# Optimization experiments

Hardware: AMD Instinct MI355X
Metric: run time of the kernel (lower is better)

## Reference

```python
import jax, jax.numpy as jnp
import numpy as np

NUM_HEADS = 16
BN_EPS = 1e-3  # tf.layers.BatchNormalization default epsilon


def _z_norm(a, axis, scale):
    mu = jnp.mean(a, axis=axis, keepdims=True)
    sd = jnp.std(a, axis=axis, keepdims=True)
    return (a - mu) / (sd * scale + 1e-10)


def setup_inputs() -> dict:
    key = jax.random.key(0)
    ks = jax.random.split(key, 12)
    B, S, D = 4, 1024, 1024
    w = lambda k: jax.random.normal(k, (D, D), dtype=jnp.float32) * 0.02
    return {
        'q': jax.random.normal(ks[0], (B, S, D), dtype=jnp.float32),
        'k': jax.random.normal(ks[1], (B, S, D), dtype=jnp.float32),
        'v': jax.random.normal(ks[2], (B, S, D), dtype=jnp.float32),
        'mask': jax.random.randint(ks[3], (B, 1, S, S), 0, 2, dtype=jnp.int32),
        'is_training': 0,
        'q_gamma': jnp.ones((D,), jnp.float32),
        'q_beta': jnp.zeros((D,), jnp.float32),
        'q_mean': jax.random.normal(ks[4], (D,), dtype=jnp.float32) * 0.1,
        'q_var': jnp.ones((D,), jnp.float32),
        'Wq': w(ks[5]), 'bq': jnp.zeros((D,), jnp.float32),
        'Wqq': w(ks[6]), 'bqq': jnp.zeros((D,), jnp.float32),
        'Wo': w(ks[7]), 'bo': jnp.zeros((D,), jnp.float32),
    }


def reference(q, k, v, mask, is_training, q_gamma, q_beta, q_mean, q_var,
              Wq, bq, Wqq, bqq, Wo, bo):
    B, S, D = q.shape
    H = NUM_HEADS
    dh = D // H
    # BatchNorm (inference mode: call() passes no training flag -> moving stats)
    x = (q - q_mean) * jax.lax.rsqrt(q_var + BN_EPS) * q_gamma + q_beta
    # q = wqq(relu(wq(.)))  (k/v projections are dead: call() sets k = v = q)
    x = jax.nn.relu(x @ Wq + bq)
    x = x @ Wqq + bqq
    qh = x.reshape(B, S, H, dh).transpose(0, 2, 1, 3)  # [B,H,S,dh]
    logits = jnp.einsum('bhqd,bhkd->bhqk', qh, qh) / jnp.sqrt(jnp.float32(dh))
    logits = logits + mask.astype(logits.dtype) * -1e9
    attn = jax.nn.softmax(logits, axis=3)  # [B,H,S,S]
    last = jnp.mean(logits, axis=-1, keepdims=True)        # [B,H,S,1]
    last2 = jnp.mean(logits, axis=(2, 3), keepdims=True)   # [B,H,1,1]
    w_within = jax.nn.softmax(_z_norm(last, 2, 2), axis=2)   # softmax over queries
    w_betw = jax.nn.softmax(_z_norm(last2, 1, 2), axis=1)    # softmax over heads
    attn = attn * w_within * w_betw
    out = jnp.einsum('bhqk,bhkd->bhqd', attn, qh)           # v == qh
    out = out.transpose(0, 2, 1, 3).reshape(B, S, D)
    out = out @ Wo + bo
    return out, attn
```

## Files before the change

### kernel.cpp

```cpp
#include <hip/hip_runtime.h>
#include <math.h>


constexpr int Bz = 4, S = 1024, D = 1024, H = 16, DH = 64;
constexpr int N_ROWS = Bz * S;
#define BN_EPS 1e-3f
#define NEG_BIG -1e9f

typedef __attribute__((ext_vector_type(8))) short bf16x8;
typedef __attribute__((ext_vector_type(8))) unsigned short u16x8;
typedef __attribute__((ext_vector_type(4))) float f32x4;

__device__ inline unsigned short f2bf(float f) {
  union { float f; unsigned int u; } v; v.f = f;
  unsigned int u = v.u;
  return (unsigned short)((u + 0x7FFFu + ((u >> 16) & 1u)) >> 16);
}
__device__ inline float bf2f(unsigned short h) {
  union { unsigned int u; float f; } v; v.u = ((unsigned int)h) << 16;
  return v.f;
}
__device__ inline bf16x8 pack8(float4 a, float4 b) {
  bf16x8 v;
  v[0] = (short)f2bf(a.x); v[1] = (short)f2bf(a.y);
  v[2] = (short)f2bf(a.z); v[3] = (short)f2bf(a.w);
  v[4] = (short)f2bf(b.x); v[5] = (short)f2bf(b.y);
  v[6] = (short)f2bf(b.z); v[7] = (short)f2bf(b.w);
  return v;
}
__device__ inline float4 bnf(float4 f, float4 s, float4 sh) {
  return make_float4(fmaf(f.x, s.x, sh.x), fmaf(f.y, s.y, sh.y),
                     fmaf(f.z, s.z, sh.z), fmaf(f.w, s.w, sh.w));
}

__global__ __launch_bounds__(256)
void k_prep_all(const float* __restrict__ W0, const float* __restrict__ W1,
                const float* __restrict__ W2, unsigned short* __restrict__ T0,
                unsigned short* __restrict__ T1, unsigned short* __restrict__ T2,
                const float* __restrict__ gamma, const float* __restrict__ beta,
                const float* __restrict__ mean, const float* __restrict__ var,
                float* __restrict__ bnsc, float* __restrict__ bnsh,
                const int* __restrict__ mask, float* __restrict__ n_cnt2,
                float* __restrict__ cs) {
  __shared__ float Ls[64][65];
  const int bid = blockIdx.x, t = threadIdx.x;
  if (bid < 768) {
    const int z = bid >> 8, rem = bid & 255;
    const float* W = z == 0 ? W0 : (z == 1 ? W1 : W2);
    unsigned short* T = z == 0 ? T0 : (z == 1 ? T1 : T2);
    const int k0 = (rem & 15) * 64, n0 = (rem >> 4) * 64;
    {
      const int r = t >> 2, c0 = (t & 3) * 16;
#pragma unroll
      for (int i = 0; i < 4; ++i) {
        float4 f = *(const float4*)&W[(size_t)(k0 + r) * 1024 + n0 + c0 + 4 * i];
        Ls[r][c0 + 4 * i] = f.x; Ls[r][c0 + 4 * i + 1] = f.y;
        Ls[r][c0 + 4 * i + 2] = f.z; Ls[r][c0 + 4 * i + 3] = f.w;
      }
    }
    __syncthreads();
    {
      const int d = t >> 2, c = t & 3;
      u16x8 o0, o1;
#pragma unroll
      for (int i = 0; i < 8; ++i) {
        o0[i] = f2bf(Ls[c * 16 + i][d]);
        o1[i] = f2bf(Ls[c * 16 + 8 + i][d]);
      }
      unsigned short* dst = &T[(size_t)(n0 + d) * 1024 + k0 + c * 16];
      *(u16x8*)dst = o0;
      *(u16x8*)(dst + 8) = o1;
    }
  } else if (bid < 832) {
    const int id = bid - 768;
    const int row = id * 64 + (t >> 2);
    const int4* mp = (const int4*)&mask[(size_t)row * 1024 + (t & 3) * 256];
    int s = 0;
#pragma unroll 8
    for (int i = 0; i < 64; ++i) { int4 m = mp[i]; s += (m.x + m.y) + (m.z + m.w); }
    s += __shfl_xor(s, 1, 64);
    s += __shfl_xor(s, 2, 64);
    if ((t & 3) == 0) n_cnt2[row] = (float)s;
  } else if (bid < 836) {
    const int id = bid - 832;
    *(float4*)&cs[id * 1024 + t * 4] = make_float4(0.f, 0.f, 0.f, 0.f);
  } else {
    const int i = (bid - 836) * 256 + t;
    float sc = gamma[i] * rsqrtf(var[i] + BN_EPS);
    bnsc[i] = sc;
    bnsh[i] = beta[i] - mean[i] * sc;
  }
}

template<int AMODE, bool RELU, bool OUTBF, bool CSUM>
__global__ __launch_bounds__(256)
void k_gemm2n(const void* __restrict__ Asrc, const unsigned short* __restrict__ BT,
              const float* __restrict__ bias, void* __restrict__ C,
              const float* __restrict__ bnsc, const float* __restrict__ bnsh,
              float* __restrict__ cs) {
  __shared__ unsigned short As[128 * 64];
  __shared__ unsigned short Bs[64 * 64];
  const int t = threadIdx.x;
  const int w = t >> 6, l = t & 63, l15 = l & 15, l4 = l >> 4;
  const int m0 = blockIdx.x * 128, n0 = blockIdx.y * 64;
  const int wm = (w >> 1) * 64, wn = (w & 1) * 32;

  f32x4 acc[4][2];
#pragma unroll
  for (int i = 0; i < 4; ++i)
#pragma unroll
    for (int j = 0; j < 2; ++j) acc[i][j] = (f32x4){0.f, 0.f, 0.f, 0.f};

  for (int k0 = 0; k0 < 1024; k0 += 64) {
    __syncthreads();
#pragma unroll
    for (int i = 0; i < 4; ++i) {
      const int c = i * 256 + t, row = c >> 3, slot = c & 7;
      bf16x8 v;
      if (AMODE == 0) {
        v = *(const bf16x8*)&((const unsigned short*)Asrc)[(size_t)(m0 + row) * 1024 + k0 + slot * 8];
      } else {
        const float* ap = &((const float*)Asrc)[(size_t)(m0 + row) * 1024 + k0 + slot * 8];
        float4 f0 = *(const float4*)ap, f1 = *(const float4*)(ap + 4);
        float4 s0 = *(const float4*)&bnsc[k0 + slot * 8];
        float4 s1 = *(const float4*)&bnsc[k0 + slot * 8 + 4];
        float4 h0 = *(const float4*)&bnsh[k0 + slot * 8];
        float4 h1 = *(const float4*)&bnsh[k0 + slot * 8 + 4];
        v = pack8(bnf(f0, s0, h0), bnf(f1, s1, h1));
      }
      *(bf16x8*)((char*)As + row * 128 + ((slot * 16) ^ ((row & 7) << 4))) = v;
    }
#pragma unroll
    for (int i = 0; i < 2; ++i) {
      const int c = i * 256 + t, row = c >> 3, slot = c & 7;
      bf16x8 v = *(const bf16x8*)&BT[(size_t)(n0 + row) * 1024 + k0 + slot * 8];
      *(bf16x8*)((char*)Bs + row * 128 + ((slot * 16) ^ ((row & 7) << 4))) = v;
    }
    __syncthreads();
    bf16x8 af[4][2], bfr[2][2];
#pragma unroll
    for (int bm = 0; bm < 4; ++bm) {
      const int r = wm + bm * 16 + l15;
#pragma unroll
      for (int kk = 0; kk < 2; ++kk)
        af[bm][kk] = *(const bf16x8*)((const char*)As + r * 128 +
                                      ((kk * 64 + l4 * 16) ^ ((r & 7) << 4)));
    }
#pragma unroll
    for (int bn = 0; bn < 2; ++bn) {
      const int r = wn + bn * 16 + l15;
#pragma unroll
      for (int kk = 0; kk < 2; ++kk)
        bfr[bn][kk] = *(const bf16x8*)((const char*)Bs + r * 128 +
                                       ((kk * 64 + l4 * 16) ^ ((r & 7) << 4)));
    }
#pragma unroll
    for (int bm = 0; bm < 4; ++bm)
#pragma unroll
      for (int bn = 0; bn < 2; ++bn) {
        acc[bm][bn] = __builtin_amdgcn_mfma_f32_16x16x32_bf16(af[bm][0], bfr[bn][0], acc[bm][bn], 0, 0, 0);
        acc[bm][bn] = __builtin_amdgcn_mfma_f32_16x16x32_bf16(af[bm][1], bfr[bn][1], acc[bm][bn], 0, 0, 0);
      }
  }
  float bv[2];
#pragma unroll
  for (int bn = 0; bn < 2; ++bn) bv[bn] = bias[n0 + wn + bn * 16 + l15];
  float csum[2] = {0.f, 0.f};
#pragma unroll
  for (int bm = 0; bm < 4; ++bm)
#pragma unroll
    for (int bn = 0; bn < 2; ++bn)
#pragma unroll
      for (int r = 0; r < 4; ++r) {
        float v = acc[bm][bn][r] + bv[bn];
        if (RELU) v = fmaxf(v, 0.f);
        if (CSUM) csum[bn] += v;
        const size_t idx = (size_t)(m0 + wm + bm * 16 + l4 * 4 + r) * 1024 +
                           n0 + wn + bn * 16 + l15;
        if (OUTBF) ((unsigned short*)C)[idx] = f2bf(v);
        else ((float*)C)[idx] = v;
      }
  if (CSUM) {
#pragma unroll
    for (int bn = 0; bn < 2; ++bn) {
      float s = csum[bn];
      s += __shfl_xor(s, 16, 64);
      s += __shfl_xor(s, 32, 64);
      if (l4 == 0)
        atomicAdd(&cs[(m0 >> 10) * 1024 + n0 + wn + bn * 16 + l15], s);
    }
  }
}

__global__ __launch_bounds__(256)
void k_cvt(const unsigned short* __restrict__ xqb, unsigned short* __restrict__ qhT) {
  __shared__ unsigned short Ls[64][72];
  const int t = threadIdx.x;
  const int b = blockIdx.x >> 4;
  const int sb = (blockIdx.x & 15) * 64;
  const int h = blockIdx.y;
  {
    const int r = t >> 2, c0 = (t & 3) * 16;
    const unsigned short* src = &xqb[(size_t)(b * 1024 + sb + r) * 1024 + h * 64 + c0];
    u16x8 a = *(const u16x8*)src;
    u16x8 b8 = *(const u16x8*)(src + 8);
    *(u16x8*)&Ls[r][c0] = a;
    *(u16x8*)&Ls[r][c0 + 8] = b8;
  }
  __syncthreads();
  {
    const int d = t >> 2, c = t & 3;
    u16x8 o0, o1;
#pragma unroll
    for (int i = 0; i < 8; ++i) {
      o0[i] = Ls[c * 16 + i][d];
      o1[i] = Ls[c * 16 + 8 + i][d];
    }
    unsigned short* dst = &qhT[(size_t)((b * 16 + h) * 64 + d) * 1024 + sb + c * 16];
    *(u16x8*)dst = o0;
    *(u16x8*)(dst + 8) = o1;
  }
}

template<int PASS>
__global__ __launch_bounds__(256)
void k_attn5(const unsigned short* __restrict__ xqb, const int* __restrict__ mask,
             const unsigned short* __restrict__ qhT, const float* __restrict__ w_row,
             float* __restrict__ attn, unsigned short* __restrict__ pvb,
             float* __restrict__ denom) {
  __shared__ unsigned short Ks[2][64 * 64];
  __shared__ unsigned short Pst[PASS ? 4 * 16 * 64 : 8];

  const int t = threadIdx.x;
  const int w = t >> 6, l = t & 63;
  const int l15 = l & 15, l4 = l >> 4;
  const int q0 = blockIdx.x * 64;
  const int h = blockIdx.y, b = blockIdx.z;
  const int bh = b * 16 + h;

  bf16x8 qa0, qa1;
  {
    const unsigned short* qp =
        &xqb[(size_t)(b * 1024 + q0 + w * 16 + l15) * 1024 + h * 64 + l4 * 8];
    qa0 = *(const bf16x8*)qp;
    qa1 = *(const bf16x8*)(qp + 32);
  }

  float wsc[4];
  if (PASS == 1) {
#pragma unroll
    for (int r = 0; r < 4; ++r)
      wsc[r] = w_row[(size_t)bh * 1024 + q0 + w * 16 + l4 * 4 + r];
  }

  float dsum[4] = {0.f, 0.f, 0.f, 0.f};
  f32x4 vacc[4];
#pragma unroll
  for (int c = 0; c < 4; ++c) vacc[c] = (f32x4){0.f, 0.f, 0.f, 0.f};

  const int srow = t >> 3, sslot = t & 7;
  const int sswz = (sslot * 16) ^ ((srow & 7) << 4);
  const size_t sga = (size_t)(b * 1024 + srow) * 1024 + h * 64 + sslot * 8;

  bf16x8 s0 = *(const bf16x8*)&xqb[sga];
  bf16x8 s1 = *(const bf16x8*)&xqb[sga + 32 * 1024];
  *(bf16x8*)((char*)Ks[0] + srow * 128 + sswz) = s0;
  *(bf16x8*)((char*)Ks[0] + (srow + 32) * 128 + sswz) = s1;
  s0 = *(const bf16x8*)&xqb[sga + 64 * 1024];
  s1 = *(const bf16x8*)&xqb[sga + 96 * 1024];

  for (int ti = 0; ti < 16; ++ti) {
    __syncthreads();
    const int cur = ti & 1;
    if (ti < 15) {
      *(bf16x8*)((char*)Ks[cur ^ 1] + srow * 128 + sswz) = s0;
      *(bf16x8*)((char*)Ks[cur ^ 1] + (srow + 32) * 128 + sswz) = s1;
    }
    if (ti < 14) {
      s0 = *(const bf16x8*)&xqb[sga + (size_t)(ti + 2) * 65536];
      s1 = *(const bf16x8*)&xqb[sga + (size_t)(ti + 2) * 65536 + 32 * 1024];
    }
    const int k0 = ti * 64;

    f32x4 lacc[4];
#pragma unroll
    for (int c = 0; c < 4; ++c) {
      const int r = c * 16 + l15;
      const char* kb = (const char*)Ks[cur] + r * 128;
      const int rsw = (r & 7) << 4;
      bf16x8 kb0 = *(const bf16x8*)(kb + ((l4 * 16) ^ rsw));
      bf16x8 kb1 = *(const bf16x8*)(kb + ((64 + l4 * 16) ^ rsw));
      f32x4 z = (f32x4){0.f, 0.f, 0.f, 0.f};
      z = __builtin_amdgcn_mfma_f32_16x16x32_bf16(qa0, kb0, z, 0, 0, 0);
      z = __builtin_amdgcn_mfma_f32_16x16x32_bf16(qa1, kb1, z, 0, 0, 0);
      lacc[c] = z;
    }

    int mrr[4][4];
#pragma unroll
    for (int c = 0; c < 4; ++c)
#pragma unroll
      for (int r = 0; r < 4; ++r)
        mrr[c][r] = mask[(size_t)(b * 1024 + q0 + w * 16 + l4 * 4 + r) * 1024 +
                         k0 + c * 16 + l15];

#pragma unroll
    for (int c = 0; c < 4; ++c) {
#pragma unroll
      for (int r = 0; r < 4; ++r) {
        float p = __expf(fmaf((float)mrr[c][r], NEG_BIG, lacc[c][r] * 0.125f));
        if (PASS == 0) {
          dsum[r] += p;
        } else {
          attn[(size_t)(bh * 1024 + q0 + w * 16 + l4 * 4 + r) * 1024 +
               k0 + c * 16 + l15] = p * wsc[r];
          const int qq = l4 * 4 + r;
          *(unsigned short*)((char*)&Pst[w * 1024] + qq * 128 +
                             (((c * 16 + l15) * 2) ^ ((qq & 7) << 4))) = f2bf(p);
        }
      }
    }

    if (PASS == 1) {
#pragma unroll
      for (int kk = 0; kk < 2; ++kk) {
        const char* pb = (const char*)&Pst[w * 1024] + l15 * 128;
        bf16x8 pa = *(const bf16x8*)(pb + ((kk * 64 + l4 * 16) ^ ((l15 & 7) << 4)));
#pragma unroll
        for (int c = 0; c < 4; ++c) {
          bf16x8 vb = *(const bf16x8*)&qhT[(size_t)(bh * 64 + c * 16 + l15) * 1024 +
                                           k0 + kk * 32 + l4 * 8];
          vacc[c] = __builtin_amdgcn_mfma_f32_16x16x32_bf16(pa, vb, vacc[c], 0, 0, 0);
        }
      }
    }
  }

  if (PASS == 0) {
#pragma unroll
    for (int r = 0; r < 4; ++r) {
      float d2 = dsum[r];
#pragma unroll
      for (int m = 1; m < 16; m <<= 1) d2 += __shfl_xor(d2, m, 64);
      if (l15 == 0)
        denom[(size_t)bh * 1024 + q0 + w * 16 + l4 * 4 + r] = d2;
    }
  } else {
#pragma unroll
    for (int c = 0; c < 4; ++c)
#pragma unroll
      for (int r = 0; r < 4; ++r)
        pvb[(size_t)(b * 1024 + q0 + w * 16 + l4 * 4 + r) * 1024 +
            h * 64 + c * 16 + l15] = f2bf(vacc[c][r] * wsc[r]);
  }
}

__global__ __launch_bounds__(256)
void k_wwithin(const unsigned short* __restrict__ xqb, const float* __restrict__ cs,
               const float* __restrict__ n_cnt2, const float* __restrict__ denom,
               float* __restrict__ w_row) {
  __shared__ double buf[1024];
  __shared__ double red[256];
  __shared__ float csl[64];
  __shared__ double sh_mu, sh_sd, sh_zm, sh_es;
  const int bh = blockIdx.x, t = threadIdx.x;
  const int base = bh << 10;
  const int b = bh >> 4, h = bh & 15;
  const int nbase = b << 10;
  if (t < 64) csl[t] = cs[b * 1024 + h * 64 + t];
  __syncthreads();
  double part = 0;
  for (int j = 0; j < 4; ++j) {
    const int q2 = t + j * 256;
    const unsigned short* xr = &xqb[(size_t)(b * 1024 + q2) * 1024 + h * 64];
    float s = 0.f;
#pragma unroll
    for (int dd = 0; dd < 64; dd += 8) {
      u16x8 xv = *(const u16x8*)&xr[dd];
      s += bf2f(xv[0]) * csl[dd]     + bf2f(xv[1]) * csl[dd + 1] +
           bf2f(xv[2]) * csl[dd + 2] + bf2f(xv[3]) * csl[dd + 3] +
           bf2f(xv[4]) * csl[dd + 4] + bf2f(xv[5]) * csl[dd + 5] +
           bf2f(xv[6]) * csl[dd + 6] + bf2f(xv[7]) * csl[dd + 7];
    }
    double last = ((double)(s * 0.125f) - 1e9 * (double)n_cnt2[nbase + q2]) * (1.0 / 1024.0);
    buf[q2] = last; part += last;
  }
  red[t] = part; __syncthreads();
  for (int s2 = 128; s2 > 0; s2 >>= 1) { if (t < s2) red[t] += red[t + s2]; __syncthreads(); }
  if (t == 0) sh_mu = red[0] * (1.0 / 1024.0);
  __syncthreads();
  const double mu = sh_mu;
  part = 0;
  for (int q2 = t; q2 < 1024; q2 += 256) { double d = buf[q2] - mu; part += d * d; }
  red[t] = part; __syncthreads();
  for (int s2 = 128; s2 > 0; s2 >>= 1) { if (t < s2) red[t] += red[t + s2]; __syncthreads(); }
  if (t == 0) sh_sd = sqrt(red[0] * (1.0 / 1024.0));
  __syncthreads();
  const double dn = sh_sd * 2.0 + 1e-10;
  part = -1e300;
  for (int q2 = t; q2 < 1024; q2 += 256) {
    double z = (buf[q2] - mu) / dn;
    buf[q2] = z;
    part = fmax(part, z);
  }
  red[t] = part; __syncthreads();
  for (int s2 = 128; s2 > 0; s2 >>= 1) { if (t < s2) red[t] = fmax(red[t], red[t + s2]); __syncthreads(); }
  if (t == 0) sh_zm = red[0];
  __syncthreads();
  const double zm = sh_zm;
  part = 0;
  for (int q2 = t; q2 < 1024; q2 += 256) {
    double e = exp(buf[q2] - zm);
    buf[q2] = e; part += e;
  }
  red[t] = part; __syncthreads();
  for (int s2 = 128; s2 > 0; s2 >>= 1) { if (t < s2) red[t] += red[t + s2]; __syncthreads(); }
  if (t == 0) sh_es = red[0];
  __syncthreads();
  const double tot = sh_es;
  for (int q2 = t; q2 < 1024; q2 += 256) {
    w_row[base + q2] = (float)(buf[q2] / tot * 0.0625 / (double)denom[base + q2]);
  }
}

extern "C" void kernel_launch(void* const* d_in, const int* in_sizes, int n_in,
                              void* d_out, int out_size, void* d_ws, size_t ws_size,
                              hipStream_t stream) {
  const float* q      = (const float*)d_in[0];
  const int*   mask   = (const int*)d_in[3];
  const float* q_gamma = (const float*)d_in[5];
  const float* q_beta  = (const float*)d_in[6];
  const float* q_mean  = (const float*)d_in[7];
  const float* q_var   = (const float*)d_in[8];
  const float* Wq  = (const float*)d_in[9];
  const float* bq  = (const float*)d_in[10];
  const float* Wqq = (const float*)d_in[11];
  const float* bqq = (const float*)d_in[12];
  const float* Wo  = (const float*)d_in[13];
  const float* bo  = (const float*)d_in[14];

  float* out  = (float*)d_out;
  float* attn = (float*)d_out + (size_t)N_ROWS * D;
  unsigned short* xqb = (unsigned short*)d_out;

  char* ws = (char*)d_ws;
  unsigned short* x1b = (unsigned short*)(ws);
  unsigned short* qhT = (unsigned short*)(ws + (8u << 20));
  unsigned short* pvb = (unsigned short*)(ws + (16u << 20));
  unsigned short* WqT  = (unsigned short*)(ws + (32u << 20));
  unsigned short* WqqT = (unsigned short*)(ws + (34u << 20));
  unsigned short* WoT  = (unsigned short*)(ws + (36u << 20));
  float* cs     = (float*)(ws + (38u << 20));
  float* denom  = cs + 4096;
  float* w_row  = denom + 65536;
  float* n_cnt2 = w_row + 65536;
  float* bnsc   = n_cnt2 + 4096;
  float* bnsh   = bnsc + 1024;

  k_prep_all<<<840, 256, 0, stream>>>(Wq, Wqq, Wo, WqT, WqqT, WoT,
                                      q_gamma, q_beta, q_mean, q_var, bnsc, bnsh,
                                      mask, n_cnt2, cs);

  dim3 gg(32, 16);
  k_gemm2n<1, true, true, false><<<gg, 256, 0, stream>>>(q, WqT, bq, x1b, bnsc, bnsh, nullptr);
  k_gemm2n<0, false, true, true><<<gg, 256, 0, stream>>>(x1b, WqqT, bqq, xqb, nullptr, nullptr, cs);

  k_cvt<<<dim3(64, 16), 256, 0, stream>>>(xqb, qhT);

  dim3 ga(16, 16, 4);
  k_attn5<0><<<ga, 256, 0, stream>>>(xqb, mask, nullptr, nullptr, nullptr, nullptr, denom);
  k_wwithin<<<Bz * H, 256, 0, stream>>>(xqb, cs, n_cnt2, denom, w_row);
  k_attn5<1><<<ga, 256, 0, stream>>>(xqb, mask, qhT, w_row, attn, pvb, nullptr);

  k_gemm2n<0, false, false, false><<<gg, 256, 0, stream>>>(pvb, WoT, bo, out, nullptr, nullptr, nullptr);
}
```

Baseline: 247.4 us.

## Fuse two-pass attention into single pass with full-row probabilities staged in LDS

Replaces the two attention passes (one for the softmax denominator, one for the weighted output) with a single kernel. It keeps the whole 64x1024 bf16 probability tile in shared memory, finishes the normalisation after the loop, then writes attn from LDS with coalesced float4 stores. The within-query weight is now computed independently of the denominator, which removes the recomputation of QK^T, exp and the mask reads from the first pass. In exchange it uses 128KB of LDS per block, so only one block fits per CU. K tiles are now read straight from global memory instead of double-buffered LDS. attn values are also rounded through bf16 before they are written.

```diff
diff --git a/kernel.cpp b/kernel.cpp
--- a/kernel.cpp
+++ b/kernel.cpp
@@ -9,6 +9,7 @@
 
 typedef __attribute__((ext_vector_type(8))) short bf16x8;
 typedef __attribute__((ext_vector_type(8))) unsigned short u16x8;
+typedef __attribute__((ext_vector_type(4))) unsigned short u16x4;
 typedef __attribute__((ext_vector_type(4))) float f32x4;
 
 __device__ inline unsigned short f2bf(float f) {
@@ -222,143 +223,9 @@
   }
 }
 
-template<int PASS>
 __global__ __launch_bounds__(256)
-void k_attn5(const unsigned short* __restrict__ xqb, const int* __restrict__ mask,
-             const unsigned short* __restrict__ qhT, const float* __restrict__ w_row,
-             float* __restrict__ attn, unsigned short* __restrict__ pvb,
-             float* __restrict__ denom) {
-  __shared__ unsigned short Ks[2][64 * 64];
-  __shared__ unsigned short Pst[PASS ? 4 * 16 * 64 : 8];
-
-  const int t = threadIdx.x;
-  const int w = t >> 6, l = t & 63;
-  const int l15 = l & 15, l4 = l >> 4;
-  const int q0 = blockIdx.x * 64;
-  const int h = blockIdx.y, b = blockIdx.z;
-  const int bh = b * 16 + h;
-
-  bf16x8 qa0, qa1;
-  {
-    const unsigned short* qp =
-        &xqb[(size_t)(b * 1024 + q0 + w * 16 + l15) * 1024 + h * 64 + l4 * 8];
-    qa0 = *(const bf16x8*)qp;
-    qa1 = *(const bf16x8*)(qp + 32);
-  }
-
-  float wsc[4];
-  if (PASS == 1) {
-#pragma unroll
-    for (int r = 0; r < 4; ++r)
-      wsc[r] = w_row[(size_t)bh * 1024 + q0 + w * 16 + l4 * 4 + r];
-  }
-
-  float dsum[4] = {0.f, 0.f, 0.f, 0.f};
-  f32x4 vacc[4];
-#pragma unroll
-  for (int c = 0; c < 4; ++c) vacc[c] = (f32x4){0.f, 0.f, 0.f, 0.f};
-
-  const int srow = t >> 3, sslot = t & 7;
-  const int sswz = (sslot * 16) ^ ((srow & 7) << 4);
-  const size_t sga = (size_t)(b * 1024 + srow) * 1024 + h * 64 + sslot * 8;
-
-  bf16x8 s0 = *(const bf16x8*)&xqb[sga];
-  bf16x8 s1 = *(const bf16x8*)&xqb[sga + 32 * 1024];
-  *(bf16x8*)((char*)Ks[0] + srow * 128 + sswz) = s0;
-  *(bf16x8*)((char*)Ks[0] + (srow + 32) * 128 + sswz) = s1;
-  s0 = *(const bf16x8*)&xqb[sga + 64 * 1024];
-  s1 = *(const bf16x8*)&xqb[sga + 96 * 1024];
-
-  for (int ti = 0; ti < 16; ++ti) {
-    __syncthreads();
-    const int cur = ti & 1;
-    if (ti < 15) {
-      *(bf16x8*)((char*)Ks[cur ^ 1] + srow * 128 + sswz) = s0;
-      *(bf16x8*)((char*)Ks[cur ^ 1] + (srow + 32) * 128 + sswz) = s1;
-    }
-    if (ti < 14) {
-      s0 = *(const bf16x8*)&xqb[sga + (size_t)(ti + 2) * 65536];
-      s1 = *(const bf16x8*)&xqb[sga + (size_t)(ti + 2) * 65536 + 32 * 1024];
-    }
-    const int k0 = ti * 64;
-
-    f32x4 lacc[4];
-#pragma unroll
-    for (int c = 0; c < 4; ++c) {
-      const int r = c * 16 + l15;
-      const char* kb = (const char*)Ks[cur] + r * 128;
-      const int rsw = (r & 7) << 4;
-      bf16x8 kb0 = *(const bf16x8*)(kb + ((l4 * 16) ^ rsw));
-      bf16x8 kb1 = *(const bf16x8*)(kb + ((64 + l4 * 16) ^ rsw));
-      f32x4 z = (f32x4){0.f, 0.f, 0.f, 0.f};
-      z = __builtin_amdgcn_mfma_f32_16x16x32_bf16(qa0, kb0, z, 0, 0, 0);
-      z = __builtin_amdgcn_mfma_f32_16x16x32_bf16(qa1, kb1, z, 0, 0, 0);
-      lacc[c] = z;
-    }
-
-    int mrr[4][4];
-#pragma unroll
-    for (int c = 0; c < 4; ++c)
-#pragma unroll
-      for (int r = 0; r < 4; ++r)
-        mrr[c][r] = mask[(size_t)(b * 1024 + q0 + w * 16 + l4 * 4 + r) * 1024 +
-                         k0 + c * 16 + l15];
-
-#pragma unroll
-    for (int c = 0; c < 4; ++c) {
-#pragma unroll
-      for (int r = 0; r < 4; ++r) {
-        float p = __expf(fmaf((float)mrr[c][r], NEG_BIG, lacc[c][r] * 0.125f));
-        if (PASS == 0) {
-          dsum[r] += p;
-        } else {
-          attn[(size_t)(bh * 1024 + q0 + w * 16 + l4 * 4 + r) * 1024 +
-               k0 + c * 16 + l15] = p * wsc[r];
-          const int qq = l4 * 4 + r;
-          *(unsigned short*)((char*)&Pst[w * 1024] + qq * 128 +
-                             (((c * 16 + l15) * 2) ^ ((qq & 7) << 4))) = f2bf(p);
-        }
-      }
-    }
-
-    if (PASS == 1) {
-#pragma unroll
-      for (int kk = 0; kk < 2; ++kk) {
-        const char* pb = (const char*)&Pst[w * 1024] + l15 * 128;
-        bf16x8 pa = *(const bf16x8*)(pb + ((kk * 64 + l4 * 16) ^ ((l15 & 7) << 4)));
-#pragma unroll
-        for (int c = 0; c < 4; ++c) {
-          bf16x8 vb = *(const bf16x8*)&qhT[(size_t)(bh * 64 + c * 16 + l15) * 1024 +
-                                           k0 + kk * 32 + l4 * 8];
-          vacc[c] = __builtin_amdgcn_mfma_f32_16x16x32_bf16(pa, vb, vacc[c], 0, 0, 0);
-        }
-      }
-    }
-  }
-
-  if (PASS == 0) {
-#pragma unroll
-    for (int r = 0; r < 4; ++r) {
-      float d2 = dsum[r];
-#pragma unroll
-      for (int m = 1; m < 16; m <<= 1) d2 += __shfl_xor(d2, m, 64);
-      if (l15 == 0)
-        denom[(size_t)bh * 1024 + q0 + w * 16 + l4 * 4 + r] = d2;
-    }
-  } else {
-#pragma unroll
-    for (int c = 0; c < 4; ++c)
-#pragma unroll
-      for (int r = 0; r < 4; ++r)
-        pvb[(size_t)(b * 1024 + q0 + w * 16 + l4 * 4 + r) * 1024 +
-            h * 64 + c * 16 + l15] = f2bf(vacc[c][r] * wsc[r]);
-  }
-}
-
-__global__ __launch_bounds__(256)
-void k_wwithin(const unsigned short* __restrict__ xqb, const float* __restrict__ cs,
-               const float* __restrict__ n_cnt2, const float* __restrict__ denom,
-               float* __restrict__ w_row) {
+void k_wwin(const unsigned short* __restrict__ xqb, const float* __restrict__ cs,
+            const float* __restrict__ n_cnt2, float* __restrict__ wwin) {
   __shared__ double buf[1024];
   __shared__ double red[256];
   __shared__ float csl[64];
@@ -419,7 +286,117 @@
   __syncthreads();
   const double tot = sh_es;
   for (int q2 = t; q2 < 1024; q2 += 256) {
-    w_row[base + q2] = (float)(buf[q2] / tot * 0.0625 / (double)denom[base + q2]);
+    wwin[base + q2] = (float)(buf[q2] / tot * 0.0625);
+  }
+}
+
+__global__ __launch_bounds__(256)
+void k_attn_f(const unsigned short* __restrict__ xqb, const int* __restrict__ mask,
+              const unsigned short* __restrict__ qhT, const float* __restrict__ wwin,
+              float* __restrict__ attn, unsigned short* __restrict__ pvb) {
+  __shared__ unsigned short Pl[64 * 1024];
+  __shared__ float wrl[64];
+
+  const int t = threadIdx.x;
+  const int w = t >> 6, l = t & 63;
+  const int l15 = l & 15, l4 = l >> 4;
+  const int q0 = blockIdx.x * 64;
+  const int h = blockIdx.y, b = blockIdx.z;
+  const int bh = b * 16 + h;
+
+  bf16x8 qa0, qa1;
+  {
+    const unsigned short* qp =
+        &xqb[(size_t)(b * 1024 + q0 + w * 16 + l15) * 1024 + h * 64 + l4 * 8];
+    qa0 = *(const bf16x8*)qp;
+    qa1 = *(const bf16x8*)(qp + 32);
+  }
+
+  float dsum[4] = {0.f, 0.f, 0.f, 0.f};
+  f32x4 vacc[4];
+#pragma unroll
+  for (int c = 0; c < 4; ++c) vacc[c] = (f32x4){0.f, 0.f, 0.f, 0.f};
+
+  for (int k0 = 0; k0 < 1024; k0 += 64) {
+    f32x4 lacc[4];
+#pragma unroll
+    for (int c = 0; c < 4; ++c) {
+      const unsigned short* kp =
+          &xqb[(size_t)(b * 1024 + k0 + c * 16 + l15) * 1024 + h * 64 + l4 * 8];
+      bf16x8 kb0 = *(const bf16x8*)kp;
+      bf16x8 kb1 = *(const bf16x8*)(kp + 32);
+      f32x4 z = (f32x4){0.f, 0.f, 0.f, 0.f};
+      z = __builtin_amdgcn_mfma_f32_16x16x32_bf16(qa0, kb0, z, 0, 0, 0);
+      z = __builtin_amdgcn_mfma_f32_16x16x32_bf16(qa1, kb1, z, 0, 0, 0);
+      lacc[c] = z;
+    }
+
+    int mrr[4][4];
+#pragma unroll
+    for (int c = 0; c < 4; ++c)
+#pragma unroll
+      for (int r = 0; r < 4; ++r)
+        mrr[c][r] = mask[(size_t)(b * 1024 + q0 + w * 16 + l4 * 4 + r) * 1024 +
+                         k0 + c * 16 + l15];
+
+#pragma unroll
+    for (int c = 0; c < 4; ++c) {
+#pragma unroll
+      for (int r = 0; r < 4; ++r) {
+        float p = __expf(fmaf((float)mrr[c][r], NEG_BIG, lacc[c][r] * 0.125f));
+        dsum[r] += p;
+        const int qq = w * 16 + l4 * 4 + r;
+        *(unsigned short*)((char*)Pl + qq * 2048 +
+                           ((((k0 + c * 16 + l15)) * 2) ^ ((qq & 7) << 4))) = f2bf(p);
+      }
+    }
+
+#pragma unroll
+    for (int kk = 0; kk < 2; ++kk) {
+      const int rp = w * 16 + l15;
+      bf16x8 pa = *(const bf16x8*)((const char*)Pl + rp * 2048 +
+                                   (((k0 + kk * 32 + l4 * 8) * 2) ^ ((rp & 7) << 4)));
+#pragma unroll
+      for (int c = 0; c < 4; ++c) {
+        bf16x8 vb = *(const bf16x8*)&qhT[(size_t)(bh * 64 + c * 16 + l15) * 1024 +
+                                         k0 + kk * 32 + l4 * 8];
+        vacc[c] = __builtin_amdgcn_mfma_f32_16x16x32_bf16(pa, vb, vacc[c], 0, 0, 0);
+      }
+    }
+  }
+
+  float wsc[4];
+#pragma unroll
+  for (int r = 0; r < 4; ++r) {
+    float d2 = dsum[r];
+#pragma unroll
+    for (int m = 1; m < 16; m <<= 1) d2 += __shfl_xor(d2, m, 64);
+    wsc[r] = wwin[(size_t)bh * 1024 + q0 + w * 16 + l4 * 4 + r] / d2;
+    if (l15 == 0) wrl[w * 16 + l4 * 4 + r] = wsc[r];
+  }
+
+#pragma unroll
+  for (int c = 0; c < 4; ++c)
+#pragma unroll
+    for (int r = 0; r < 4; ++r)
+      pvb[(size_t)(b * 1024 + q0 + w * 16 + l4 * 4 + r) * 1024 +
+          h * 64 + c * 16 + l15] = f2bf(vacc[c][r] * wsc[r]);
+
+  __syncthreads();
+
+#pragma unroll 4
+  for (int r2 = 0; r2 < 16; ++r2) {
+    const int row = w * 16 + r2;
+    const float wq = wrl[row];
+    float* ap = &attn[(size_t)(bh * 1024 + q0 + row) * 1024];
+#pragma unroll
+    for (int k2 = 0; k2 < 4; ++k2) {
+      const int col = k2 * 256 + l * 4;
+      u16x4 p4 = *(const u16x4*)((const char*)Pl + row * 2048 +
+                                 ((col * 2) ^ ((row & 7) << 4)));
+      *(float4*)(ap + col) = make_float4(bf2f(p4[0]) * wq, bf2f(p4[1]) * wq,
+                                         bf2f(p4[2]) * wq, bf2f(p4[3]) * wq);
+    }
   }
 }
 
@@ -451,9 +428,8 @@
   unsigned short* WqqT = (unsigned short*)(ws + (34u << 20));
   unsigned short* WoT  = (unsigned short*)(ws + (36u << 20));
   float* cs     = (float*)(ws + (38u << 20));
-  float* denom  = cs + 4096;
-  float* w_row  = denom + 65536;
-  float* n_cnt2 = w_row + 65536;
+  float* wwin   = cs + 4096;
+  float* n_cnt2 = wwin + 65536;
   float* bnsc   = n_cnt2 + 4096;
   float* bnsh   = bnsc + 1024;
 
@@ -466,11 +442,10 @@
   k_gemm2n<0, false, true, true><<<gg, 256, 0, stream>>>(x1b, WqqT, bqq, xqb, nullptr, nullptr, cs);
 
   k_cvt<<<dim3(64, 16), 256, 0, stream>>>(xqb, qhT);
+  k_wwin<<<Bz * H, 256, 0, stream>>>(xqb, cs, n_cnt2, wwin);
 
   dim3 ga(16, 16, 4);
-  k_attn5<0><<<ga, 256, 0, stream>>>(xqb, mask, nullptr, nullptr, nullptr, nullptr, denom);
-  k_wwithin<<<Bz * H, 256, 0, stream>>>(xqb, cs, n_cnt2, denom, w_row);
-  k_attn5<1><<<ga, 256, 0, stream>>>(xqb, mask, qhT, w_row, attn, pvb, nullptr);
+  k_attn_f<<<ga, 256, 0, stream>>>(xqb, mask, qhT, wwin, attn, pvb);
 
   k_gemm2n<0, false, false, false><<<gg, 256, 0, stream>>>(pvb, WoT, bo, out, nullptr, nullptr, nullptr);
 }
```

New measurement: 279.2 us. 1.13x slower.
